# Kernel tuning notes

Hardware: AMD Instinct MI355X
Metric: run time of the kernel (lower is better)

Reference implementation:

```python
import jax, jax.numpy as jnp
import numpy as np

N_MODELS = 16
IN_F = 1024
OUT_F = 1024
N_TOK = 8192


def setup_inputs() -> dict:
    key = jax.random.key(0)
    k1, k2, k3, k4 = jax.random.split(key, 4)
    x = jax.random.normal(k1, (N_TOK, IN_F), dtype=jnp.float32)
    idxs = jax.random.randint(k2, (N_TOK,), 0, N_MODELS, dtype=jnp.int64)
    w = jax.random.normal(k3, (N_MODELS, IN_F, OUT_F), dtype=jnp.float32) * 0.02
    b = jax.random.normal(k4, (N_MODELS, OUT_F), dtype=jnp.float32) * 0.02
    return {"x": x, "idxs": idxs, "w": w, "b": b}


def reference(x, idxs, w, b):
    # Equivalent math to the torch loop: for each expert i, tokens with
    # idxs==i get x @ w[i] + b[i]; finally ReLU over all outputs.
    # Loop over the small fixed expert count; selection by mask avoids
    # materializing the [N, E, out] tensor or gathering per-token weights.
    y = jnp.zeros((x.shape[0], w.shape[2]), dtype=x.dtype)
    for i in range(w.shape[0]):
        yi = x @ w[i] + b[i]  # [N, out]
        y = jnp.where((idxs == i)[:, None], yi, y)
    return jax.nn.relu(y)
```

## Files before the change

### kernel.cpp

```cpp
#include <hip/hip_runtime.h>
#include <hip/hip_bf16.h>
#include <stdint.h>

#define N_MODELS 16
#define IN_F 1024
#define OUT_F 1024
#define N_TOK 8192
#define MAX_MT 80

typedef unsigned short u16;
using us4   = __attribute__((ext_vector_type(4))) unsigned short;
using s16x8 = __attribute__((ext_vector_type(8))) short;
using f32x4 = __attribute__((ext_vector_type(4))) float;

__device__ __forceinline__ u16 f2bf(float f) {
    union { float f; uint32_t u; } v;
    v.f = f;
    uint32_t u = v.u;
    u += 0x7fffu + ((u >> 16) & 1u);
    return (u16)(u >> 16);
}

__device__ __forceinline__ void gload16(const u16* g, u16* l) {
    __builtin_amdgcn_global_load_lds(
        (const __attribute__((address_space(1))) void*)g,
        (__attribute__((address_space(3))) void*)l, 16, 0, 0);
}

#define ROW 17
#define WBLOCKS 2048

__global__ __launch_bounds__(256)
void wprep_setup_kernel(const float* __restrict__ w,
                        const int* __restrict__ idxs,
                        int* __restrict__ perm,
                        int* __restrict__ offs,
                        int* __restrict__ tile_off,
                        u16* __restrict__ wT)
{
    __shared__ int cnt[256 * ROW];
    __shared__ int offsS[N_MODELS + 1];
    int t  = threadIdx.x;
    int bx = blockIdx.x;

    if (bx == 0) {
#pragma unroll
        for (int e = 0; e < N_MODELS; ++e) cnt[t * ROW + e] = 0;
        __syncthreads();

        int base = t * 32;
#pragma unroll
        for (int i = 0; i < 32; ++i) cnt[t * ROW + idxs[base + i]] += 1;
        __syncthreads();

#pragma unroll
        for (int s = 1; s < 256; s <<= 1) {
            int v[N_MODELS];
#pragma unroll
            for (int e = 0; e < N_MODELS; ++e)
                v[e] = (t >= s) ? cnt[(t - s) * ROW + e] : 0;
            __syncthreads();
#pragma unroll
            for (int e = 0; e < N_MODELS; ++e)
                cnt[t * ROW + e] += v[e];
            __syncthreads();
        }

        if (t == 0) {
            int o = 0, to = 0;
            for (int e = 0; e < N_MODELS; ++e) {
                int c = cnt[255 * ROW + e];
                offsS[e] = o;
                offs[e] = o; tile_off[e] = to;
                to += (c + 127) >> 7;
                o  += c;
            }
            offsS[N_MODELS] = o;
            offs[N_MODELS] = o; tile_off[N_MODELS] = to;
        }
        __syncthreads();

        int cur[N_MODELS];
#pragma unroll
        for (int e = 0; e < N_MODELS; ++e)
            cur[e] = offsS[e] + ((t > 0) ? cnt[(t - 1) * ROW + e] : 0);
        __syncthreads();
#pragma unroll
        for (int e = 0; e < N_MODELS; ++e) cnt[t * ROW + e] = cur[e];

#pragma unroll
        for (int i = 0; i < 32; ++i) {
            int tok = base + i;
            int e = idxs[tok];
            perm[cnt[t * ROW + e]++] = tok;
        }
        return;
    }

    int wb = bx - 1;
    int e  = wb >> 7;
    int nt = (wb >> 4) & 7;
    int kg = wb & 15;
    int n    = t & 127;
    int half = t >> 7;

    const float* wp = w  + (size_t)e * (IN_F * OUT_F) + (size_t)nt * 128 + n;
    u16*         ob = wT + ((size_t)(e * 8 + nt)) * 131072 + (size_t)n * 8;

#pragma unroll
    for (int i = 0; i < 4; ++i) {
        int kog = kg * 8 + half + i * 2;
        float r[8];
#pragma unroll
        for (int j = 0; j < 8; ++j)
            r[j] = wp[(size_t)(kog * 8 + j) * OUT_F];
        union { __hip_bfloat162 h; uint32_t u; } c0, c1, c2, c3;
        c0.h = __float22bfloat162_rn(make_float2(r[0], r[1]));
        c1.h = __float22bfloat162_rn(make_float2(r[2], r[3]));
        c2.h = __float22bfloat162_rn(make_float2(r[4], r[5]));
        c3.h = __float22bfloat162_rn(make_float2(r[6], r[7]));
        union { s16x8 v; uint32_t u[4]; } outv;
        outv.u[0] = c0.u; outv.u[1] = c1.u; outv.u[2] = c2.u; outv.u[3] = c3.u;
        *(s16x8*)(ob + (size_t)kog * 1024) = outv.v;
    }
}

#define XBLOCKS (MAX_MT * 8)

__global__ __launch_bounds__(256)
void xprep_kernel(const float* __restrict__ x,
                  const int* __restrict__ perm, const int* __restrict__ offs,
                  const int* __restrict__ tile_off,
                  u16* __restrict__ xg)
{
    int t  = threadIdx.x;
    int bx = blockIdx.x;
    int mt = bx >> 3;
    int kg = bx & 7;
    int total = tile_off[N_MODELS];
    if (mt >= total) return;
    int e = 0;
    while (tile_off[e + 1] <= mt) ++e;
    int s0   = offs[e] + (mt - tile_off[e]) * 128;
    int sEnd = offs[e + 1];

    int r0   = t >> 3;
    int apos = t & 7;
    int q    = apos >> 1;
    int j0   = (apos & 1) * 4;

    int toks[4];
#pragma unroll
    for (int i = 0; i < 4; ++i) {
        int r = r0 + i * 32;
        toks[i] = (s0 + r < sEnd) ? perm[s0 + r] : -1;
    }

    u16* outx = xg + (size_t)mt * 131072;
#pragma unroll
    for (int kb4 = 0; kb4 < 4; ++kb4) {
        int kb = kg * 4 + kb4;
        int k  = kb * 32 + apos * 4;
#pragma unroll
        for (int i = 0; i < 4; ++i) {
            int r = r0 + i * 32;
            float4 v;
            if (toks[i] >= 0) v = *(const float4*)(x + (size_t)toks[i] * IN_F + k);
            else              v = make_float4(0.f, 0.f, 0.f, 0.f);
            us4 pk; pk.x = f2bf(v.x); pk.y = f2bf(v.y); pk.z = f2bf(v.z); pk.w = f2bf(v.w);
            *(us4*)(outx + (size_t)kb * 4096 + (size_t)q * 1024 + r * 8 + j0) = pk;
        }
    }
}

__global__ __launch_bounds__(256)
void gemm_kernel(const u16* __restrict__ xg, const u16* __restrict__ wT,
                 const float* __restrict__ bias,
                 const int* __restrict__ perm, const int* __restrict__ offs,
                 const int* __restrict__ tile_off,
                 float* __restrict__ out)
{
    __shared__ u16 As[8192];
    __shared__ u16 Bs[8192];
    __shared__ int   permS[128];
    __shared__ float biasS[128];
    __shared__ int   toS[N_MODELS + 1];

    int t = threadIdx.x;
    int o    = blockIdx.x;
    int wgid = (o & 7) * MAX_MT + (o >> 3);
    int bt   = wgid >> 3;
    int nt   = wgid & 7;

    if (t <= N_MODELS) toS[t] = tile_off[t];
    __syncthreads();
    if (bt >= toS[N_MODELS]) return;

    int e = 0;
    while (toS[e + 1] <= bt) ++e;
    int s0   = offs[e] + (bt - toS[e]) * 128;
    int sEnd = offs[e + 1];
    int mValid = sEnd - s0; if (mValid > 128) mValid = 128;

    if (t < 128) {
        permS[t] = (s0 + t < sEnd) ? perm[s0 + t] : 0;
        biasS[t] = bias[(size_t)e * OUT_F + nt * 128 + t];
    }

    const u16* atile = xg + (size_t)bt * 32 * 4096;
    const u16* btile = wT + ((size_t)(e * 8 + nt)) * 131072;

    int lane = t & 63;
    int wv   = t >> 6;
    int wm   = (wv >> 1) * 64;
    int wn   = (wv & 1) * 64;
    int m    = lane & 15;
    int q    = lane >> 4;

    f32x4 acc[4][4];
#pragma unroll
    for (int i = 0; i < 4; ++i)
#pragma unroll
        for (int j = 0; j < 4; ++j)
            acc[i][j] = (f32x4){0.f, 0.f, 0.f, 0.f};

    int c = wv * 2;

    for (int kb2 = 0; kb2 < 16; ++kb2) {
        const u16* ga = atile + kb2 * 8192;
        const u16* gb = btile + kb2 * 8192;
        gload16(ga + (c    ) * 512 + lane * 8, &As[(c    ) * 512]);
        gload16(ga + (c + 1) * 512 + lane * 8, &As[(c + 1) * 512]);
        gload16(ga + 4096 + (c    ) * 512 + lane * 8, &As[4096 + (c    ) * 512]);
        gload16(ga + 4096 + (c + 1) * 512 + lane * 8, &As[4096 + (c + 1) * 512]);
        gload16(gb + (c    ) * 512 + lane * 8, &Bs[(c    ) * 512]);
        gload16(gb + (c + 1) * 512 + lane * 8, &Bs[(c + 1) * 512]);
        gload16(gb + 4096 + (c    ) * 512 + lane * 8, &Bs[4096 + (c    ) * 512]);
        gload16(gb + 4096 + (c + 1) * 512 + lane * 8, &Bs[4096 + (c + 1) * 512]);
        __syncthreads();

#pragma unroll
        for (int s = 0; s < 2; ++s) {
            s16x8 af[4], bf[4];
#pragma unroll
            for (int mt2 = 0; mt2 < 4; ++mt2)
                af[mt2] = *(const s16x8*)(&As[s * 4096 + q * 1024 + (wm + mt2 * 16 + m) * 8]);
#pragma unroll
            for (int nt2 = 0; nt2 < 4; ++nt2)
                bf[nt2] = *(const s16x8*)(&Bs[s * 4096 + q * 1024 + (wn + nt2 * 16 + m) * 8]);
#pragma unroll
            for (int mt2 = 0; mt2 < 4; ++mt2)
#pragma unroll
                for (int nt2 = 0; nt2 < 4; ++nt2)
                    acc[mt2][nt2] = __builtin_amdgcn_mfma_f32_16x16x32_bf16(
                        af[mt2], bf[nt2], acc[mt2][nt2], 0, 0, 0);
        }
        __syncthreads();
    }

#pragma unroll
    for (int mt2 = 0; mt2 < 4; ++mt2) {
        int rbase = wm + mt2 * 16 + q * 4;
#pragma unroll
        for (int i = 0; i < 4; ++i) {
            int r = rbase + i;
            if (r < mValid) {
                int tok = permS[r];
                float* orow = out + (size_t)tok * OUT_F + nt * 128;
#pragma unroll
                for (int nt2 = 0; nt2 < 4; ++nt2) {
                    int col = wn + nt2 * 16 + m;
                    float v = acc[mt2][nt2][i] + biasS[col];
                    orow[col] = v > 0.f ? v : 0.f;
                }
            }
        }
    }
}

extern "C" void kernel_launch(void* const* d_in, const int* in_sizes, int n_in,
                              void* d_out, int out_size, void* d_ws, size_t ws_size,
                              hipStream_t stream) {
    const float* x    = (const float*)d_in[0];
    const int*   idxs = (const int*)d_in[1];
    const float* w    = (const float*)d_in[2];
    const float* b    = (const float*)d_in[3];
    float* out = (float*)d_out;

    u16* wT = (u16*)d_ws;
    u16* xg = wT + (size_t)N_MODELS * IN_F * OUT_F;
    int* perm     = (int*)(xg + (size_t)MAX_MT * 32 * 4096);
    int* offs     = perm + N_TOK;
    int* tile_off = offs + (N_MODELS + 1);

    wprep_setup_kernel<<<WBLOCKS + 1, 256, 0, stream>>>(w, idxs, perm, offs, tile_off, wT);
    xprep_kernel<<<XBLOCKS, 256, 0, stream>>>(x, perm, offs, tile_off, xg);
    gemm_kernel<<<8 * MAX_MT, 256, 0, stream>>>(xg, wT, b, perm, offs, tile_off, out);
}
```

Baseline: 180.6 us.

## Double-buffer B tile in LDS and stream A fragments directly into registers

The GEMM kernel stops staging the A (token) tile through shared memory. Each wave now loads its A fragments straight from global memory into registers, prefetching the next k-slice while the current one runs through MFMA. The B (weight) tile is double-buffered in LDS, so the next slice loads asynchronously during compute, and only one barrier per iteration remains. This aims to overlap global loads with MFMA work and cut LDS traffic, at the cost of more VGPRs (an occupancy hint of 3 is added) and uncoalesced-per-wave global reads for A that are duplicated across the two N-waves.

```diff
diff --git a/kernel.cpp b/kernel.cpp
--- a/kernel.cpp
+++ b/kernel.cpp
@@ -173,15 +173,14 @@
     }
 }
 
-__global__ __launch_bounds__(256)
+__global__ __launch_bounds__(256, 3)
 void gemm_kernel(const u16* __restrict__ xg, const u16* __restrict__ wT,
                  const float* __restrict__ bias,
                  const int* __restrict__ perm, const int* __restrict__ offs,
                  const int* __restrict__ tile_off,
                  float* __restrict__ out)
 {
-    __shared__ u16 As[8192];
-    __shared__ u16 Bs[8192];
+    __shared__ u16 Bs[2][8192];
     __shared__ int   permS[128];
     __shared__ float biasS[128];
     __shared__ int   toS[N_MODELS + 1];
@@ -207,7 +206,7 @@
         biasS[t] = bias[(size_t)e * OUT_F + nt * 128 + t];
     }
 
-    const u16* atile = xg + (size_t)bt * 32 * 4096;
+    const u16* atile = xg + (size_t)bt * 131072;
     const u16* btile = wT + ((size_t)(e * 8 + nt)) * 131072;
 
     int lane = t & 63;
@@ -217,6 +216,9 @@
     int m    = lane & 15;
     int q    = lane >> 4;
 
+    int aoff = q * 1024 + (wm + m) * 8;
+    int boff = q * 1024 + (wn + m) * 8;
+
     f32x4 acc[4][4];
 #pragma unroll
     for (int i = 0; i < 4; ++i)
@@ -224,38 +226,60 @@
         for (int j = 0; j < 4; ++j)
             acc[i][j] = (f32x4){0.f, 0.f, 0.f, 0.f};
 
-    int c = wv * 2;
+#pragma unroll
+    for (int i = 0; i < 4; ++i)
+        gload16(btile + wv * 2048 + i * 512 + lane * 8, &Bs[0][wv * 2048 + i * 512]);
+
+    s16x8 a0[4], a1[4];
+#pragma unroll
+    for (int mt2 = 0; mt2 < 4; ++mt2)
+        a0[mt2] = *(const s16x8*)(atile + aoff + mt2 * 128);
+#pragma unroll
+    for (int mt2 = 0; mt2 < 4; ++mt2)
+        a1[mt2] = *(const s16x8*)(atile + 4096 + aoff + mt2 * 128);
 
     for (int kb2 = 0; kb2 < 16; ++kb2) {
-        const u16* ga = atile + kb2 * 8192;
-        const u16* gb = btile + kb2 * 8192;
-        gload16(ga + (c    ) * 512 + lane * 8, &As[(c    ) * 512]);
-        gload16(ga + (c + 1) * 512 + lane * 8, &As[(c + 1) * 512]);
-        gload16(ga + 4096 + (c    ) * 512 + lane * 8, &As[4096 + (c    ) * 512]);
-        gload16(ga + 4096 + (c + 1) * 512 + lane * 8, &As[4096 + (c + 1) * 512]);
-        gload16(gb + (c    ) * 512 + lane * 8, &Bs[(c    ) * 512]);
-        gload16(gb + (c + 1) * 512 + lane * 8, &Bs[(c + 1) * 512]);
-        gload16(gb + 4096 + (c    ) * 512 + lane * 8, &Bs[4096 + (c    ) * 512]);
-        gload16(gb + 4096 + (c + 1) * 512 + lane * 8, &Bs[4096 + (c + 1) * 512]);
-        __syncthreads();
-
-#pragma unroll
-        for (int s = 0; s < 2; ++s) {
-            s16x8 af[4], bf[4];
+        int cur = kb2 & 1;
+        __syncthreads();
+        if (kb2 < 15) {
+            const u16* gb = btile + (size_t)(kb2 + 1) * 8192;
+#pragma unroll
+            for (int i = 0; i < 4; ++i)
+                gload16(gb + wv * 2048 + i * 512 + lane * 8,
+                        &Bs[cur ^ 1][wv * 2048 + i * 512]);
+        }
+        if (kb2 > 0) {
 #pragma unroll
             for (int mt2 = 0; mt2 < 4; ++mt2)
-                af[mt2] = *(const s16x8*)(&As[s * 4096 + q * 1024 + (wm + mt2 * 16 + m) * 8]);
+                a1[mt2] = *(const s16x8*)(atile + (size_t)kb2 * 8192 + 4096 + aoff + mt2 * 128);
+        }
+
+        s16x8 bf[4];
+#pragma unroll
+        for (int nt2 = 0; nt2 < 4; ++nt2)
+            bf[nt2] = *(const s16x8*)(&Bs[cur][boff + nt2 * 128]);
+#pragma unroll
+        for (int mt2 = 0; mt2 < 4; ++mt2)
 #pragma unroll
             for (int nt2 = 0; nt2 < 4; ++nt2)
-                bf[nt2] = *(const s16x8*)(&Bs[s * 4096 + q * 1024 + (wn + nt2 * 16 + m) * 8]);
+                acc[mt2][nt2] = __builtin_amdgcn_mfma_f32_16x16x32_bf16(
+                    a0[mt2], bf[nt2], acc[mt2][nt2], 0, 0, 0);
+
+        if (kb2 < 15) {
 #pragma unroll
             for (int mt2 = 0; mt2 < 4; ++mt2)
-#pragma unroll
-                for (int nt2 = 0; nt2 < 4; ++nt2)
-                    acc[mt2][nt2] = __builtin_amdgcn_mfma_f32_16x16x32_bf16(
-                        af[mt2], bf[nt2], acc[mt2][nt2], 0, 0, 0);
-        }
-        __syncthreads();
+                a0[mt2] = *(const s16x8*)(atile + (size_t)(kb2 + 1) * 8192 + aoff + mt2 * 128);
+        }
+
+#pragma unroll
+        for (int nt2 = 0; nt2 < 4; ++nt2)
+            bf[nt2] = *(const s16x8*)(&Bs[cur][4096 + boff + nt2 * 128]);
+#pragma unroll
+        for (int mt2 = 0; mt2 < 4; ++mt2)
+#pragma unroll
+            for (int nt2 = 0; nt2 < 4; ++nt2)
+                acc[mt2][nt2] = __builtin_amdgcn_mfma_f32_16x16x32_bf16(
+                    a1[mt2], bf[nt2], acc[mt2][nt2], 0, 0, 0);
     }
 
 #pragma unroll
```

Measured after the change: 180.0 us. Within noise of the previous version (-0.3%).

## Load A fragments directly to registers and double-buffer B in LDS

Applied to the files above, without the earlier changes.

The GEMM main loop stops staging A through shared memory. Each wave now loads its A fragments straight from global memory into registers, with a register ping-pong prefetch of the next k-block. B is double-buffered in LDS so the next tile's asynchronous load overlaps the current MFMAs, leaving one barrier per iteration instead of two. Launch bounds now request 3 waves per EU, which trades register pressure (roughly 128 extra VGPRs for A fragments) against occupancy. A rows are shared by only two waves, so the global A loads are duplicated across waves.

```diff
diff --git a/kernel.cpp b/kernel.cpp
--- a/kernel.cpp
+++ b/kernel.cpp
@@ -173,15 +173,14 @@
     }
 }
 
-__global__ __launch_bounds__(256)
+__global__ __launch_bounds__(256, 3)
 void gemm_kernel(const u16* __restrict__ xg, const u16* __restrict__ wT,
                  const float* __restrict__ bias,
                  const int* __restrict__ perm, const int* __restrict__ offs,
                  const int* __restrict__ tile_off,
                  float* __restrict__ out)
 {
-    __shared__ u16 As[8192];
-    __shared__ u16 Bs[8192];
+    __shared__ u16 Bs[2][8192];
     __shared__ int   permS[128];
     __shared__ float biasS[128];
     __shared__ int   toS[N_MODELS + 1];
@@ -207,7 +206,7 @@
         biasS[t] = bias[(size_t)e * OUT_F + nt * 128 + t];
     }
 
-    const u16* atile = xg + (size_t)bt * 32 * 4096;
+    const u16* atile = xg + (size_t)bt * 131072;
     const u16* btile = wT + ((size_t)(e * 8 + nt)) * 131072;
 
     int lane = t & 63;
@@ -217,6 +216,9 @@
     int m    = lane & 15;
     int q    = lane >> 4;
 
+    int aoff = q * 1024 + (wm + m) * 8;
+    int boff = q * 1024 + (wn + m) * 8;
+
     f32x4 acc[4][4];
 #pragma unroll
     for (int i = 0; i < 4; ++i)
@@ -224,39 +226,67 @@
         for (int j = 0; j < 4; ++j)
             acc[i][j] = (f32x4){0.f, 0.f, 0.f, 0.f};
 
-    int c = wv * 2;
-
-    for (int kb2 = 0; kb2 < 16; ++kb2) {
-        const u16* ga = atile + kb2 * 8192;
-        const u16* gb = btile + kb2 * 8192;
-        gload16(ga + (c    ) * 512 + lane * 8, &As[(c    ) * 512]);
-        gload16(ga + (c + 1) * 512 + lane * 8, &As[(c + 1) * 512]);
-        gload16(ga + 4096 + (c    ) * 512 + lane * 8, &As[4096 + (c    ) * 512]);
-        gload16(ga + 4096 + (c + 1) * 512 + lane * 8, &As[4096 + (c + 1) * 512]);
-        gload16(gb + (c    ) * 512 + lane * 8, &Bs[(c    ) * 512]);
-        gload16(gb + (c + 1) * 512 + lane * 8, &Bs[(c + 1) * 512]);
-        gload16(gb + 4096 + (c    ) * 512 + lane * 8, &Bs[4096 + (c    ) * 512]);
-        gload16(gb + 4096 + (c + 1) * 512 + lane * 8, &Bs[4096 + (c + 1) * 512]);
-        __syncthreads();
-
-#pragma unroll
-        for (int s = 0; s < 2; ++s) {
-            s16x8 af[4], bf[4];
-#pragma unroll
-            for (int mt2 = 0; mt2 < 4; ++mt2)
-                af[mt2] = *(const s16x8*)(&As[s * 4096 + q * 1024 + (wm + mt2 * 16 + m) * 8]);
-#pragma unroll
-            for (int nt2 = 0; nt2 < 4; ++nt2)
-                bf[nt2] = *(const s16x8*)(&Bs[s * 4096 + q * 1024 + (wn + nt2 * 16 + m) * 8]);
-#pragma unroll
-            for (int mt2 = 0; mt2 < 4; ++mt2)
-#pragma unroll
-                for (int nt2 = 0; nt2 < 4; ++nt2)
-                    acc[mt2][nt2] = __builtin_amdgcn_mfma_f32_16x16x32_bf16(
-                        af[mt2], bf[nt2], acc[mt2][nt2], 0, 0, 0);
-        }
-        __syncthreads();
-    }
+#pragma unroll
+    for (int i = 0; i < 4; ++i)
+        gload16(btile + wv * 2048 + i * 512 + lane * 8, &Bs[0][wv * 2048 + i * 512]);
+
+    s16x8 aA0[4], aA1[4], aB0[4], aB1[4];
+#pragma unroll
+    for (int mt2 = 0; mt2 < 4; ++mt2)
+        aA0[mt2] = *(const s16x8*)(atile + aoff + mt2 * 128);
+#pragma unroll
+    for (int mt2 = 0; mt2 < 4; ++mt2)
+        aA1[mt2] = *(const s16x8*)(atile + 4096 + aoff + mt2 * 128);
+
+#define GEMM_STEP(kb2, aIn0, aIn1, aOut0, aOut1)                                       \
+    {                                                                                   \
+        int cur = (kb2) & 1;                                                            \
+        __syncthreads();                 \
+        if ((kb2) < 15) {                                                               \
+            const u16* gb = btile + (size_t)((kb2) + 1) * 8192;                         \
+            _Pragma("unroll")                                                           \
+            for (int i = 0; i < 4; ++i)                                                 \
+                gload16(gb + wv * 2048 + i * 512 + lane * 8,                            \
+                        &Bs[cur ^ 1][wv * 2048 + i * 512]);                             \
+        }                                                                               \
+                                                                  \
+        s16x8 bf[4];                                                                    \
+        _Pragma("unroll")                                                               \
+        for (int nt2 = 0; nt2 < 4; ++nt2)                                               \
+            bf[nt2] = *(const s16x8*)(&Bs[cur][boff + nt2 * 128]);                      \
+        _Pragma("unroll")                                                               \
+        for (int mt2 = 0; mt2 < 4; ++mt2)                                               \
+            _Pragma("unroll")                                                           \
+            for (int nt2 = 0; nt2 < 4; ++nt2)                                           \
+                acc[mt2][nt2] = __builtin_amdgcn_mfma_f32_16x16x32_bf16(                \
+                    aIn0[mt2], bf[nt2], acc[mt2][nt2], 0, 0, 0);                        \
+        if ((kb2) < 15) {    \
+            _Pragma("unroll")                                                           \
+            for (int mt2 = 0; mt2 < 4; ++mt2)                                           \
+                aOut0[mt2] = *(const s16x8*)(atile + (size_t)((kb2) + 1) * 8192         \
+                                             + aoff + mt2 * 128);                       \
+            _Pragma("unroll")                                                           \
+            for (int mt2 = 0; mt2 < 4; ++mt2)                                           \
+                aOut1[mt2] = *(const s16x8*)(atile + (size_t)((kb2) + 1) * 8192 + 4096  \
+                                             + aoff + mt2 * 128);                       \
+        }                                                                               \
+                                                                  \
+        _Pragma("unroll")                                                               \
+        for (int nt2 = 0; nt2 < 4; ++nt2)                                               \
+            bf[nt2] = *(const s16x8*)(&Bs[cur][4096 + boff + nt2 * 128]);               \
+        _Pragma("unroll")                                                               \
+        for (int mt2 = 0; mt2 < 4; ++mt2)                                               \
+            _Pragma("unroll")                                                           \
+            for (int nt2 = 0; nt2 < 4; ++nt2)                                           \
+                acc[mt2][nt2] = __builtin_amdgcn_mfma_f32_16x16x32_bf16(                \
+                    aIn1[mt2], bf[nt2], acc[mt2][nt2], 0, 0, 0);                        \
+    }
+
+    for (int kb2 = 0; kb2 < 16; kb2 += 2) {
+        GEMM_STEP(kb2,     aA0, aA1, aB0, aB1);
+        GEMM_STEP(kb2 + 1, aB0, aB1, aA0, aA1);
+    }
+#undef GEMM_STEP
 
 #pragma unroll
     for (int mt2 = 0; mt2 < 4; ++mt2) {
```

After: 180.9 us. Within noise of the previous version (+0.2%).
